# Optimization experiments

Hardware: AMD Instinct MI355X
Metric: run time of the kernel (lower is better)

## Reference

```python
import jax, jax.numpy as jnp
import numpy as np

B, N, D, H = 2048, 200, 128, 8

def setup_inputs() -> dict:
    key = jax.random.key(0)
    k1, k2, k3, k4, k5, k6 = jax.random.split(key, 6)
    return {
        "item_embedding": jax.random.normal(k1, (B, N, D), dtype=jnp.float32),
        "query_embedding": jax.random.normal(k2, (B, D), dtype=jnp.float32),
        "mask": jax.random.randint(k3, (B, N, 1), 0, 2).astype(bool),
        "Wq": jax.random.normal(k4, (D * H, D), dtype=jnp.float32) * 0.05,
        "bq": jax.random.normal(k5, (D * H,), dtype=jnp.float32) * 0.05,
        "Wr": jax.random.normal(k6, (1, H), dtype=jnp.float32) * 0.5,
    }

def reference(item_embedding, query_embedding, mask, Wq, bq, Wr):
    b = query_embedding.shape[0]
    # query projection + tanh, reshape to (B, D, H)
    pq = jnp.tanh(query_embedding @ Wq.T + bq).reshape(b, D, H)
    # batched dot: (B,N,D) @ (B,D,H) -> (B,N,H)
    dotted = jnp.einsum('bnd,bdh->bnh', item_embedding, pq)
    # head reduce: (B,N,H) @ (H,1) -> (B,N,1)
    reduced = dotted @ Wr.T
    scores = reduced - jnp.max(reduced, axis=1, keepdims=True)
    att = jnp.exp(scores) * mask
    denom = jnp.sum(att, axis=1, keepdims=True)
    weight = att / jnp.where(denom < 1e-7, denom + 1.0, denom)
    # weighted sum pooling -> (B, D)
    return jnp.sum(weight * item_embedding, axis=1)
```

## Files before the change

### kernel.cpp

```cpp
#include <hip/hip_runtime.h>

#define BB 2048
#define NN 200
#define DD 128
#define HH 8

typedef float f4v __attribute__((ext_vector_type(4)));

__global__ __launch_bounds__(256) void proj_kernel(
    const float* __restrict__ q,
    const float* __restrict__ Wq,
    const float* __restrict__ bq,
    const float* __restrict__ Wr,
    float* __restrict__ v)
{
    __shared__ float wq_s[32][257];
    const int t  = threadIdx.x;
    const int jc = blockIdx.x;
    const int b0 = blockIdx.y * 16;
    const int j  = jc * 256 + t;

    float acc[16];
#pragma unroll
    for (int i = 0; i < 16; ++i) acc[i] = 0.f;

    for (int kt = 0; kt < 4; ++kt) {
        __syncthreads();
#pragma unroll
        for (int i = 0; i < 8; ++i) {
            int idx = t + 256 * i;
            int jj  = idx >> 3;
            int kf  = idx & 7;
            const float4 w4 = *(const float4*)(Wq + (size_t)(jc*256 + jj)*128 + kt*32 + kf*4);
            wq_s[kf*4+0][jj] = w4.x;
            wq_s[kf*4+1][jj] = w4.y;
            wq_s[kf*4+2][jj] = w4.z;
            wq_s[kf*4+3][jj] = w4.w;
        }
        __syncthreads();

        float wreg[32];
#pragma unroll
        for (int k = 0; k < 32; ++k) wreg[k] = wq_s[k][t];

#pragma unroll
        for (int bb = 0; bb < 16; ++bb) {
            const float* qrow = q + (size_t)(b0 + bb)*128 + kt*32;
            float s = 0.f;
#pragma unroll
            for (int k = 0; k < 32; ++k) s = fmaf(qrow[k], wreg[k], s);
            acc[bb] += s;
        }
    }

    const float bqj = bq[j];
    const float wrh = Wr[j & 7];
    const int   d   = j >> 3;
#pragma unroll
    for (int bb = 0; bb < 16; ++bb) {
        float p = tanhf(acc[bb] + bqj) * wrh;
        p += __shfl_xor(p, 1);
        p += __shfl_xor(p, 2);
        p += __shfl_xor(p, 4);
        if ((t & 7) == 0) v[(size_t)(b0 + bb)*128 + d] = p;
    }
}

__global__ __launch_bounds__(512, 8) void attn_kernel(
    const float* __restrict__ item,
    const int*   __restrict__ mask,
    const float* __restrict__ v,
    float* __restrict__ out)
{
    __shared__ float  mask_s[NN];
    __shared__ float2 ml_s[16];
    __shared__ __align__(16) float stage[16][132];

    const int t    = threadIdx.x;
    const int b    = blockIdx.x;
    const int seg  = t & 31;
    const int half = t >> 5;

    const f4v vreg = *(const f4v*)(v + (size_t)b*128 + seg*4);
    const float* itemb = item + (size_t)b * (NN * 128);

    if (t < NN) mask_s[t] = mask[(size_t)b * NN + t] ? 1.f : 0.f;

    f4v pre[5];
#pragma unroll
    for (int i = 0; i < 5; ++i) {
        const int row = half + 16*i;
        pre[i] = (f4v)0.f;
        if (row < 64)
            pre[i] = __builtin_nontemporal_load(
                (const f4v*)(itemb + (size_t)row*128 + seg*4));
    }
    __syncthreads();

    float mh = -3e38f, lh = 0.f;
    f4v oh = (f4v)0.f;

    for (int c = 0; c < 3; ++c) {
        const int base = c * 64;
        const int rows = (c == 2) ? 72 : 64;

        float pp[5];
#pragma unroll
        for (int i = 0; i < 5; ++i) {
            const f4v f = pre[i];
            float s = f[0]*vreg[0] + f[1]*vreg[1] + f[2]*vreg[2] + f[3]*vreg[3];
#pragma unroll
            for (int off = 16; off >= 1; off >>= 1)
                s += __shfl_xor(s, off);
            pp[i] = s;
        }

        float mn = mh;
#pragma unroll
        for (int i = 0; i < 5; ++i)
            if (half + 16*i < rows) mn = fmaxf(mn, pp[i]);

        const float alpha = __expf(mh - mn);
        mh = mn;
        lh *= alpha;
        oh[0] *= alpha; oh[1] *= alpha; oh[2] *= alpha; oh[3] *= alpha;

#pragma unroll
        for (int i = 0; i < 5; ++i) {
            const int row = half + 16*i;
            if (row < rows) {
                const float w = mask_s[base + row] * __expf(pp[i] - mn);
                lh += w;
                oh[0] = fmaf(w, pre[i][0], oh[0]);
                oh[1] = fmaf(w, pre[i][1], oh[1]);
                oh[2] = fmaf(w, pre[i][2], oh[2]);
                oh[3] = fmaf(w, pre[i][3], oh[3]);
            }
        }

        if (c < 2) {
            const int nbase = (c + 1) * 64;
            const int nrows = (c == 1) ? 72 : 64;
#pragma unroll
            for (int i = 0; i < 5; ++i) {
                const int row = half + 16*i;
                pre[i] = (f4v)0.f;
                if (row < nrows)
                    pre[i] = __builtin_nontemporal_load(
                        (const f4v*)(itemb + (size_t)(nbase + row)*128 + seg*4));
            }
        }
    }

    if (seg == 0) ml_s[half] = make_float2(mh, lh);
    *(f4v*)(&stage[half][seg*4]) = oh;
    __syncthreads();

    if (t < 128) {
        float mg = -3e38f;
#pragma unroll
        for (int h = 0; h < 16; ++h) mg = fmaxf(mg, ml_s[h].x);
        float lsum = 0.f, tot = 0.f;
#pragma unroll
        for (int h = 0; h < 16; ++h) {
            const float sc = __expf(ml_s[h].x - mg);
            lsum += ml_s[h].y * sc;
            tot  = fmaf(stage[h][t], sc, tot);
        }
        const float denom = (lsum < 1e-7f) ? (lsum + 1.f) : lsum;
        out[(size_t)b * 128 + t] = tot / denom;
    }
}

extern "C" void kernel_launch(void* const* d_in, const int* in_sizes, int n_in,
                              void* d_out, int out_size, void* d_ws, size_t ws_size,
                              hipStream_t stream) {
    const float* item = (const float*)d_in[0];
    const float* q    = (const float*)d_in[1];
    const int*   mask = (const int*)  d_in[2];
    const float* Wq   = (const float*)d_in[3];
    const float* bq   = (const float*)d_in[4];
    const float* Wr   = (const float*)d_in[5];
    float* out = (float*)d_out;
    float* v   = (float*)d_ws;

    proj_kernel<<<dim3(4, 128), 256, 0, stream>>>(q, Wq, bq, Wr, v);
    attn_kernel<<<dim3(BB), 512, 0, stream>>>(item, mask, v, out);
}
```

Baseline: 320.1 us.

## Process two batch rows per attention block with cross-row prefetch

Each attention block now handles two consecutive batch rows instead of one, halving the grid. During the last chunk of the first row it prefetches the second row's item tiles, query vector and mask, so the load pipeline stays busy across rows. This amortizes block launch and startup latency but halves the number of blocks, which can reduce parallelism. Shared memory per block roughly doubles.

Result: slower. 332.9 us (+4.0%).

```diff
diff --git a/kernel.cpp b/kernel.cpp
--- a/kernel.cpp
+++ b/kernel.cpp
@@ -72,19 +72,23 @@
     const float* __restrict__ v,
     float* __restrict__ out)
 {
-    __shared__ float  mask_s[NN];
-    __shared__ float2 ml_s[16];
-    __shared__ __align__(16) float stage[16][132];
+    __shared__ float  mask_s[2][NN];
+    __shared__ float2 ml_s[2][16];
+    __shared__ __align__(16) float stage[2][16][132];
 
     const int t    = threadIdx.x;
-    const int b    = blockIdx.x;
     const int seg  = t & 31;
     const int half = t >> 5;
-
-    const f4v vreg = *(const f4v*)(v + (size_t)b*128 + seg*4);
-    const float* itemb = item + (size_t)b * (NN * 128);
-
-    if (t < NN) mask_s[t] = mask[(size_t)b * NN + t] ? 1.f : 0.f;
+    const int b0   = blockIdx.x * 2;
+
+    const float* itemb0 = item + (size_t)b0 * (NN * 128);
+    const int*   maskb  = mask + (size_t)b0 * NN;
+    const float* vb     = v + (size_t)b0 * 128;
+
+    if (t < NN) mask_s[0][t] = maskb[t] ? 1.f : 0.f;
+
+    f4v vreg = *(const f4v*)(vb + seg*4);
+    f4v vnext = (f4v)0.f;
 
     f4v pre[5];
 #pragma unroll
@@ -93,82 +97,95 @@
         pre[i] = (f4v)0.f;
         if (row < 64)
             pre[i] = __builtin_nontemporal_load(
-                (const f4v*)(itemb + (size_t)row*128 + seg*4));
+                (const f4v*)(itemb0 + (size_t)row*128 + seg*4));
     }
     __syncthreads();
 
-    float mh = -3e38f, lh = 0.f;
-    f4v oh = (f4v)0.f;
-
-    for (int c = 0; c < 3; ++c) {
-        const int base = c * 64;
-        const int rows = (c == 2) ? 72 : 64;
-
-        float pp[5];
-#pragma unroll
-        for (int i = 0; i < 5; ++i) {
-            const f4v f = pre[i];
-            float s = f[0]*vreg[0] + f[1]*vreg[1] + f[2]*vreg[2] + f[3]*vreg[3];
-#pragma unroll
-            for (int off = 16; off >= 1; off >>= 1)
-                s += __shfl_xor(s, off);
-            pp[i] = s;
-        }
-
-        float mn = mh;
-#pragma unroll
-        for (int i = 0; i < 5; ++i)
-            if (half + 16*i < rows) mn = fmaxf(mn, pp[i]);
-
-        const float alpha = __expf(mh - mn);
-        mh = mn;
-        lh *= alpha;
-        oh[0] *= alpha; oh[1] *= alpha; oh[2] *= alpha; oh[3] *= alpha;
-
-#pragma unroll
-        for (int i = 0; i < 5; ++i) {
-            const int row = half + 16*i;
-            if (row < rows) {
-                const float w = mask_s[base + row] * __expf(pp[i] - mn);
-                lh += w;
-                oh[0] = fmaf(w, pre[i][0], oh[0]);
-                oh[1] = fmaf(w, pre[i][1], oh[1]);
-                oh[2] = fmaf(w, pre[i][2], oh[2]);
-                oh[3] = fmaf(w, pre[i][3], oh[3]);
-            }
-        }
-
-        if (c < 2) {
-            const int nbase = (c + 1) * 64;
-            const int nrows = (c == 1) ? 72 : 64;
+#pragma unroll
+    for (int bi = 0; bi < 2; ++bi) {
+        const float* itemb = itemb0 + (size_t)bi * (NN * 128);
+
+        float mh = -3e38f, lh = 0.f;
+        f4v oh = (f4v)0.f;
+
+        for (int c = 0; c < 3; ++c) {
+            const int base = c * 64;
+            const int rows = (c == 2) ? 72 : 64;
+
+            float pp[5];
+#pragma unroll
+            for (int i = 0; i < 5; ++i) {
+                const f4v f = pre[i];
+                float s = f[0]*vreg[0] + f[1]*vreg[1] + f[2]*vreg[2] + f[3]*vreg[3];
+#pragma unroll
+                for (int off = 16; off >= 1; off >>= 1)
+                    s += __shfl_xor(s, off);
+                pp[i] = s;
+            }
+
+            float mn = mh;
+#pragma unroll
+            for (int i = 0; i < 5; ++i)
+                if (half + 16*i < rows) mn = fmaxf(mn, pp[i]);
+
+            const float alpha = __expf(mh - mn);
+            mh = mn;
+            lh *= alpha;
+            oh[0] *= alpha; oh[1] *= alpha; oh[2] *= alpha; oh[3] *= alpha;
+
 #pragma unroll
             for (int i = 0; i < 5; ++i) {
                 const int row = half + 16*i;
-                pre[i] = (f4v)0.f;
-                if (row < nrows)
-                    pre[i] = __builtin_nontemporal_load(
-                        (const f4v*)(itemb + (size_t)(nbase + row)*128 + seg*4));
-            }
-        }
-    }
-
-    if (seg == 0) ml_s[half] = make_float2(mh, lh);
-    *(f4v*)(&stage[half][seg*4]) = oh;
-    __syncthreads();
-
-    if (t < 128) {
-        float mg = -3e38f;
-#pragma unroll
-        for (int h = 0; h < 16; ++h) mg = fmaxf(mg, ml_s[h].x);
-        float lsum = 0.f, tot = 0.f;
-#pragma unroll
-        for (int h = 0; h < 16; ++h) {
-            const float sc = __expf(ml_s[h].x - mg);
-            lsum += ml_s[h].y * sc;
-            tot  = fmaf(stage[h][t], sc, tot);
-        }
-        const float denom = (lsum < 1e-7f) ? (lsum + 1.f) : lsum;
-        out[(size_t)b * 128 + t] = tot / denom;
+                if (row < rows) {
+                    const float w = mask_s[bi][base + row] * __expf(pp[i] - mn);
+                    lh += w;
+                    oh[0] = fmaf(w, pre[i][0], oh[0]);
+                    oh[1] = fmaf(w, pre[i][1], oh[1]);
+                    oh[2] = fmaf(w, pre[i][2], oh[2]);
+                    oh[3] = fmaf(w, pre[i][3], oh[3]);
+                }
+            }
+
+            const bool pf = (c < 2) || (bi == 0);
+            if (pf) {
+                const int    nbase = (c < 2) ? (c + 1) * 64 : 0;
+                const int    nrows = (c == 1) ? 72 : 64;
+                const float* nptr  = (c < 2) ? itemb : itemb0 + (size_t)(NN * 128);
+#pragma unroll
+                for (int i = 0; i < 5; ++i) {
+                    const int row = half + 16*i;
+                    pre[i] = (f4v)0.f;
+                    if (row < nrows)
+                        pre[i] = __builtin_nontemporal_load(
+                            (const f4v*)(nptr + (size_t)(nbase + row)*128 + seg*4));
+                }
+            }
+            if (bi == 0 && c == 2) {
+                vnext = *(const f4v*)(vb + 128 + seg*4);
+                if (t < NN) mask_s[1][t] = maskb[NN + t] ? 1.f : 0.f;
+            }
+        }
+
+        if (seg == 0) ml_s[bi][half] = make_float2(mh, lh);
+        *(f4v*)(&stage[bi][half][seg*4]) = oh;
+        __syncthreads();
+
+        if (t < 128) {
+            float mg = -3e38f;
+#pragma unroll
+            for (int h = 0; h < 16; ++h) mg = fmaxf(mg, ml_s[bi][h].x);
+            float lsum = 0.f, tot = 0.f;
+#pragma unroll
+            for (int h = 0; h < 16; ++h) {
+                const float sc = __expf(ml_s[bi][h].x - mg);
+                lsum += ml_s[bi][h].y * sc;
+                tot  = fmaf(stage[bi][h][t], sc, tot);
+            }
+            const float denom = (lsum < 1e-7f) ? (lsum + 1.f) : lsum;
+            out[(size_t)(b0 + bi) * 128 + t] = tot / denom;
+        }
+
+        vreg = vnext;
     }
 }
 
@@ -185,5 +202,5 @@
     float* v   = (float*)d_ws;
 
     proj_kernel<<<dim3(4, 128), 256, 0, stream>>>(q, Wq, bq, Wr, v);
-    attn_kernel<<<dim3(BB), 512, 0, stream>>>(item, mask, v, out);
+    attn_kernel<<<dim3(BB/2), 512, 0, stream>>>(item, mask, v, out);
 }
```
